# Kernel tuning notes

Measured on AMD Instinct MI355X. Metric: run time of the kernel, lower is better.

Reference implementation:

```python
import jax, jax.numpy as jnp
import numpy as np

B, S, H = 32, 64, 512
ATT = 128


def _window_index_tables(seq_len):
    # Enumerate all contiguous windows of size 2..S, same set (order-independent
    # for the softmax-weighted sum) as the torch double loop.
    starts, ends = [], []
    for w in range(2, seq_len + 1):
        for s in range(0, seq_len - w + 1):
            starts.append(s)
            ends.append(s + w)
    starts = np.asarray(starts, np.int32)
    ends = np.asarray(ends, np.int32)
    widths = ends - starts
    ks = np.floor(np.log2(widths)).astype(np.int32)  # sparse-table level per window
    e2 = ends - (1 << ks)                            # second gather position
    return starts, e2, ks


def setup_inputs() -> dict:
    key = jax.random.key(0)
    k0, k1, k2, k3, k4 = jax.random.split(key, 5)
    return {
        "lstm_out": jax.random.normal(k0, (B, S, H), dtype=jnp.float32),
        "W1": jax.random.normal(k1, (H, ATT), dtype=jnp.float32) * 0.05,
        "b1": jax.random.normal(k2, (ATT,), dtype=jnp.float32) * 0.05,
        "W2": jax.random.normal(k3, (ATT, 1), dtype=jnp.float32) * 0.05,
        "b2": jax.random.normal(k4, (1,), dtype=jnp.float32) * 0.05,
    }


def reference(lstm_out, W1, b1, W2, b2):
    b, s, h = lstm_out.shape
    # Sparse table: M[k][:, i] = max over lstm_out[:, i : i+2^k] (clipped to s).
    n_levels = int(np.floor(np.log2(s))) + 1
    tables = [lstm_out]
    for k in range(1, n_levels):
        half = 1 << (k - 1)
        prev = tables[-1]
        shifted = jnp.concatenate(
            [prev[:, half:], jnp.full((b, half, h), -jnp.inf, prev.dtype)], axis=1)
        tables.append(jnp.maximum(prev, shifted))
    Mstack = jnp.stack(tables)  # [K, B, S, H]

    starts, e2, ks = _window_index_tables(s)
    # Range max of each window = max of two overlapping power-of-two blocks.
    pooled = jnp.maximum(Mstack[ks, :, starts], Mstack[ks, :, e2])  # [n_win, B, H]
    pooled = jnp.transpose(pooled, (1, 0, 2))  # [B, n_win, H]

    hid = jax.nn.relu(jnp.einsum("bnh,ha->bna", pooled, W1) + b1)
    scores = jnp.einsum("bna,ao->bno", hid, W2) + b2  # [B, n_win, 1]
    attn = jax.nn.softmax(scores, axis=1)
    return jnp.sum(attn * pooled, axis=1)  # [B, H]
```

## Files before the change

kernel.cpp:

```cpp
#include <hip/hip_runtime.h>
#include <stdint.h>


typedef unsigned short u16;
typedef unsigned int u32;

#define B_    32
#define S_    64
#define H_    512
#define ATT_  128
#define NWIN  2016
#define NLEV  7
#define TLEV  6

typedef __bf16 bf16x8 __attribute__((ext_vector_type(8)));
typedef float  f32x4  __attribute__((ext_vector_type(4)));

__device__ __forceinline__ float asf(u32 i) {
  union { u32 i; float f; } v; v.i = i; return v.f;
}
__device__ __forceinline__ u32 asu(float f) {
  union { float f; u32 i; } v; v.f = f; return v.i;
}
__device__ __forceinline__ float bf2f(u16 u) { return asf(((u32)u) << 16); }
__device__ __forceinline__ u16 f2bf(float f) {
  u32 i = asu(f);
  i += 0x7fffu + ((i >> 16) & 1u);
  return (u16)(i >> 16);
}
__device__ __forceinline__ u32 bfmax2(u32 a, u32 b) {
  float a0 = asf(a << 16), a1 = asf(a & 0xffff0000u);
  float b0 = asf(b << 16), b1 = asf(b & 0xffff0000u);
  u32 m0 = asu(fmaxf(a0, b0)), m1 = asu(fmaxf(a1, b1));
  return (m1 & 0xffff0000u) | (m0 >> 16);
}
__device__ __forceinline__ uint4 bfmax8(uint4 a, uint4 b) {
  uint4 m;
  m.x = bfmax2(a.x, b.x); m.y = bfmax2(a.y, b.y);
  m.z = bfmax2(a.z, b.z); m.w = bfmax2(a.w, b.w);
  return m;
}
__device__ __forceinline__ bf16x8 as_bf16x8(uint4 v) {
  union { uint4 u; bf16x8 h; } c; c.u = v; return c.h;
}

__launch_bounds__(256)
__global__ void k01_init(const float* __restrict__ lstm, const float* __restrict__ W1,
                         u16* __restrict__ table, u16* __restrict__ w1t,
                         u16* __restrict__ widx) {
  int bid = blockIdx.x, tid = threadIdx.x;
  __shared__ u16 bufA[64 * 64], bufB[64 * 64];
  if (bid < 256) {
    int hc = bid & 7, b = bid >> 3;
    const float* src = lstm + (size_t)b * S_ * H_ + hc * 64;
    u16* tb = table + (size_t)b * TLEV * S_ * H_ + hc * 64;
    for (int t = tid; t < 64 * 16; t += 256) {
      int r = t >> 4, c4 = t & 15;
      float4 f = *reinterpret_cast<const float4*>(src + r * H_ + c4 * 4);
      ushort4 u;
      u.x = f2bf(f.x); u.y = f2bf(f.y); u.z = f2bf(f.z); u.w = f2bf(f.w);
      *reinterpret_cast<ushort4*>(&bufA[r * 64 + c4 * 4]) = u;
    }
    u16* pa = bufA; u16* pb = bufB;
    for (int k = 1; k < NLEV; ++k) {
      __syncthreads();
      int half = 1 << (k - 1);
      u16* dst_g = tb + (size_t)(k - 1) * S_ * H_;
      for (int t = tid; t < 64 * 16; t += 256) {
        int r = t >> 4, c4 = t & 15;
        int r2 = r + half; if (r2 > 63) r2 = 63;
        uint2 a  = *reinterpret_cast<const uint2*>(&pa[r  * 64 + c4 * 4]);
        uint2 bq = *reinterpret_cast<const uint2*>(&pa[r2 * 64 + c4 * 4]);
        uint2 m; m.x = bfmax2(a.x, bq.x); m.y = bfmax2(a.y, bq.y);
        *reinterpret_cast<uint2*>(&pb[r * 64 + c4 * 4]) = m;
        *reinterpret_cast<uint2*>(dst_g + r * H_ + c4 * 4) = m;
      }
      u16* tmp = pa; pa = pb; pb = tmp;
    }
  } else {
    int gb = bid - 256;
    if (gb == 0) {
      for (int n = tid; n < NWIN; n += 256) {
        int w = 2, rem = n;
        while (rem >= 65 - w) { rem -= 65 - w; ++w; }
        int s = rem;
        int k = 31 - __clz(w);
        int e2 = s + w - (1 << k);
        widx[n] = (u16)(s | (e2 << 6) | (k << 12));
      }
    }
    for (int q = tid; q < 2048; q += 256) {
      int idx = gb * 2048 + q;
      int n = idx >> 9, kq = idx & 511;
      w1t[idx] = f2bf(W1[kq * ATT_ + n]);
    }
  }
}

__launch_bounds__(256)
__attribute__((amdgpu_waves_per_eu(1, 4)))
__global__ void k2_scores(const u16* __restrict__ table, const u16* __restrict__ w1t,
                          const float* __restrict__ b1, const float* __restrict__ w2,
                          const u16* __restrict__ widx, float* __restrict__ scores) {
  const int b = blockIdx.y, mt = blockIdx.x;
  __shared__ u16 Ts[128 * 64];
  __shared__ u16 Bs[128 * 64];
  __shared__ u16 widx_l[64];
  __shared__ float b1s[128], w2s[128];
  int tid = threadIdx.x;
  if (tid < 64) {
    int n = mt * 64 + tid; if (n > NWIN - 1) n = NWIN - 1;
    widx_l[tid] = widx[n];
  }
  if (tid < 128) { b1s[tid] = b1[tid]; w2s[tid] = w2[tid]; }
  __syncthreads();

  const int lv_lo = widx_l[0] >> 12;
  const u16* tb = table + (size_t)b * TLEV * S_ * H_ + (size_t)(lv_lo - 1) * S_ * H_;

  int t0 = tid, t1 = tid + 256, t2 = tid + 512, t3 = tid + 768;
  int r0 = t0 >> 3, r1 = t1 >> 3, r2 = t2 >> 3, r3 = t3 >> 3;
  int c0 = t0 & 7,  c1 = t1 & 7,  c2 = t2 & 7,  c3 = t3 & 7;
  const u16* ts0 = tb + r0 * H_ + c0 * 8;
  const u16* ts1 = tb + r1 * H_ + c1 * 8;
  const u16* ts2 = tb + r2 * H_ + c2 * 8;
  const u16* ts3 = tb + r3 * H_ + c3 * 8;
  const u16* bs0 = w1t + r0 * H_ + c0 * 8;
  const u16* bs1 = w1t + r1 * H_ + c1 * 8;
  const u16* bs2 = w1t + r2 * H_ + c2 * 8;
  const u16* bs3 = w1t + r3 * H_ + c3 * 8;
  int sd0 = r0 * 64 + ((c0 ^ (r0 & 7)) * 8);
  int sd1 = r1 * 64 + ((c1 ^ (r1 & 7)) * 8);
  int sd2 = r2 * 64 + ((c2 ^ (r2 & 7)) * 8);
  int sd3 = r3 * 64 + ((c3 ^ (r3 & 7)) * 8);

  int wid = tid >> 6, lane = tid & 63;
  int lrow = lane & 15, quad = lane >> 4;

  int aoff[2][2];
  {
    int pk = widx_l[wid * 16 + lrow];
    int s = pk & 63, e2 = (pk >> 6) & 63, lv = (pk >> 12) - lv_lo;
    int rs = lv * 64 + s, re = lv * 64 + e2;
#pragma unroll
    for (int k2i = 0; k2i < 2; ++k2i) {
      int c = quad + k2i * 4;
      aoff[k2i][0] = rs * 64 + ((c ^ (rs & 7)) * 8);
      aoff[k2i][1] = re * 64 + ((c ^ (re & 7)) * 8);
    }
  }
  int boff[8][2];
#pragma unroll
  for (int j = 0; j < 8; ++j) {
    int n = j * 16 + lrow;
#pragma unroll
    for (int k2i = 0; k2i < 2; ++k2i) {
      int c = quad + k2i * 4;
      boff[j][k2i] = n * 64 + ((c ^ (n & 7)) * 8);
    }
  }

  uint4 rT0, rT1, rT2, rT3, rB0, rB1, rB2, rB3;

#define ISSUE(KK) do { \
  rT0 = *reinterpret_cast<const uint4*>(ts0 + (KK)); \
  rT1 = *reinterpret_cast<const uint4*>(ts1 + (KK)); \
  rT2 = *reinterpret_cast<const uint4*>(ts2 + (KK)); \
  rT3 = *reinterpret_cast<const uint4*>(ts3 + (KK)); \
  rB0 = *reinterpret_cast<const uint4*>(bs0 + (KK)); \
  rB1 = *reinterpret_cast<const uint4*>(bs1 + (KK)); \
  rB2 = *reinterpret_cast<const uint4*>(bs2 + (KK)); \
  rB3 = *reinterpret_cast<const uint4*>(bs3 + (KK)); \
} while (0)

#define STAGE() do { \
  *reinterpret_cast<uint4*>(&Ts[sd0]) = rT0; \
  *reinterpret_cast<uint4*>(&Ts[sd1]) = rT1; \
  *reinterpret_cast<uint4*>(&Ts[sd2]) = rT2; \
  *reinterpret_cast<uint4*>(&Ts[sd3]) = rT3; \
  *reinterpret_cast<uint4*>(&Bs[sd0]) = rB0; \
  *reinterpret_cast<uint4*>(&Bs[sd1]) = rB1; \
  *reinterpret_cast<uint4*>(&Bs[sd2]) = rB2; \
  *reinterpret_cast<uint4*>(&Bs[sd3]) = rB3; \
} while (0)

  ISSUE(0);

  f32x4 acc[8];
#pragma unroll
  for (int j = 0; j < 8; ++j) acc[j] = (f32x4){0.f, 0.f, 0.f, 0.f};

  for (int kc = 0; kc < 7; ++kc) {
    __syncthreads();
    STAGE();
    __syncthreads();
    ISSUE((kc + 1) * 64);
#pragma unroll
    for (int k2i = 0; k2i < 2; ++k2i) {
      uint4 va = *reinterpret_cast<const uint4*>(&Ts[aoff[k2i][0]]);
      uint4 vb = *reinterpret_cast<const uint4*>(&Ts[aoff[k2i][1]]);
      bf16x8 af = as_bf16x8(bfmax8(va, vb));
#pragma unroll
      for (int j = 0; j < 8; ++j) {
        bf16x8 bfr = *reinterpret_cast<const bf16x8*>(&Bs[boff[j][k2i]]);
        acc[j] = __builtin_amdgcn_mfma_f32_16x16x32_bf16(af, bfr, acc[j], 0, 0, 0);
      }
    }
  }
  __syncthreads();
  STAGE();
  __syncthreads();
#pragma unroll
  for (int k2i = 0; k2i < 2; ++k2i) {
    uint4 va = *reinterpret_cast<const uint4*>(&Ts[aoff[k2i][0]]);
    uint4 vb = *reinterpret_cast<const uint4*>(&Ts[aoff[k2i][1]]);
    bf16x8 af = as_bf16x8(bfmax8(va, vb));
#pragma unroll
    for (int j = 0; j < 8; ++j) {
      bf16x8 bfr = *reinterpret_cast<const bf16x8*>(&Bs[boff[j][k2i]]);
      acc[j] = __builtin_amdgcn_mfma_f32_16x16x32_bf16(af, bfr, acc[j], 0, 0, 0);
    }
  }

#undef ISSUE
#undef STAGE

#pragma unroll
  for (int r = 0; r < 4; ++r) {
    float p = 0.f;
#pragma unroll
    for (int j = 0; j < 8; ++j) {
      int n = j * 16 + lrow;
      float v = acc[j][r] + b1s[n];
      p += (v > 0.f ? v : 0.f) * w2s[n];
    }
    p += __shfl_xor(p, 1, 16);
    p += __shfl_xor(p, 2, 16);
    p += __shfl_xor(p, 4, 16);
    p += __shfl_xor(p, 8, 16);
    if (lrow == 0) {
      int nw = mt * 64 + wid * 16 + quad * 4 + r;
      if (nw < NWIN) scores[b * NWIN + nw] = p;
    }
  }
}

__launch_bounds__(256)
__global__ void k34_out(const u16* __restrict__ table, const float* __restrict__ scores,
                        const u16* __restrict__ widx, float* __restrict__ out) {
  int hc = blockIdx.x, b = blockIdx.y, tid = threadIdx.x;
  __shared__ u16 Tl[6 * 64 * 32];
  __shared__ float attn_l[NWIN];
  __shared__ u16 widx_l[NWIN];
  __shared__ float red[8][32];
  __shared__ float wredM[4], wredS[4];
  const u16* tb = table + (size_t)b * TLEV * S_ * H_;
  int h0 = hc * 32;
  int lane = tid & 63, wid = tid >> 6;

  for (int t = tid; t < 6 * 64 * 4; t += 256) {
    int row = t >> 2, c = t & 3;
    uint4 v = *reinterpret_cast<const uint4*>(tb + row * H_ + h0 + c * 8);
    *reinterpret_cast<uint4*>(&Tl[row * 32 + c * 8]) = v;
  }
  for (int n = tid; n < NWIN; n += 256) widx_l[n] = widx[n];

  float mx = -1e30f;
  for (int n = tid; n < NWIN; n += 256) {
    float v = scores[b * NWIN + n];
    attn_l[n] = v;
    mx = fmaxf(mx, v);
  }
#pragma unroll
  for (int off = 32; off > 0; off >>= 1) mx = fmaxf(mx, __shfl_xor(mx, off, 64));
  if (lane == 0) wredM[wid] = mx;
  __syncthreads();
  mx = fmaxf(fmaxf(wredM[0], wredM[1]), fmaxf(wredM[2], wredM[3]));
  float sum = 0.f;
  for (int n = tid; n < NWIN; n += 256) {
    float e = __expf(attn_l[n] - mx);
    attn_l[n] = e;
    sum += e;
  }
#pragma unroll
  for (int off = 32; off > 0; off >>= 1) sum += __shfl_xor(sum, off, 64);
  if (lane == 0) wredS[wid] = sum;
  __syncthreads();
  float inv = 1.f / (wredS[0] + wredS[1] + wredS[2] + wredS[3]);

  int h = tid & 31, g = tid >> 5;
  float acc = 0.f;
  for (int n = g * 252; n < g * 252 + 252; ++n) {
    int pk = widx_l[n];
    int s = pk & 63, e2 = (pk >> 6) & 63, lv = pk >> 12;
    float va = bf2f(Tl[((lv - 1) * 64 + s) * 32 + h]);
    float vb = bf2f(Tl[((lv - 1) * 64 + e2) * 32 + h]);
    acc += attn_l[n] * fmaxf(va, vb);
  }
  red[g][h] = acc;
  __syncthreads();
  if (tid < 32) {
    float s2 = 0.f;
#pragma unroll
    for (int g2 = 0; g2 < 8; ++g2) s2 += red[g2][tid];
    out[b * H_ + h0 + tid] = s2 * inv;
  }
}

extern "C" void kernel_launch(void* const* d_in, const int* in_sizes, int n_in,
                              void* d_out, int out_size, void* d_ws, size_t ws_size,
                              hipStream_t stream) {
  const float* lstm = (const float*)d_in[0];
  const float* W1   = (const float*)d_in[1];
  const float* b1   = (const float*)d_in[2];
  const float* W2   = (const float*)d_in[3];
  float* out = (float*)d_out;

  char* ws = (char*)d_ws;
  u16*   widx   = (u16*)(ws + 0);
  u16*   w1t    = (u16*)(ws + 4096);
  u16*   table  = (u16*)(ws + 135168);
  float* scores = (float*)(ws + 12718080);

  k01_init <<<288, 256, 0, stream>>>(lstm, W1, table, w1t, widx);
  k2_scores<<<dim3(32, B_), 256, 0, stream>>>(table, w1t, b1, W2, widx, scores);
  k34_out  <<<dim3(16, B_), 256, 0, stream>>>(table, scores, widx, out);
}
```

Baseline: 117.6 us.

## Enlarge score GEMM tile to 256 windows with double-buffered direct-to-LDS loads

The scores kernel now has each block cover 256 windows instead of 64. Each wave computes four 16-row M sub-tiles, so every W1 fragment read from shared memory is reused four times, and the block count falls from 32 to 8 per batch. Global-to-register-to-LDS staging is replaced by global_load_lds async copies into double-buffered shared tiles, with one barrier per K step. In exchange the accumulator count per wave grows fourfold and occupancy drops to one block per CU. Correctness relies on the async LDS copies being complete at each barrier, and on any 256-window block spanning at most two sparse-table levels.

```diff
diff --git a/kernel.cpp b/kernel.cpp
--- a/kernel.cpp
+++ b/kernel.cpp
@@ -97,19 +97,18 @@
   }
 }
 
-__launch_bounds__(256)
-__attribute__((amdgpu_waves_per_eu(1, 4)))
+__launch_bounds__(256, 1)
 __global__ void k2_scores(const u16* __restrict__ table, const u16* __restrict__ w1t,
                           const float* __restrict__ b1, const float* __restrict__ w2,
                           const u16* __restrict__ widx, float* __restrict__ scores) {
   const int b = blockIdx.y, mt = blockIdx.x;
-  __shared__ u16 Ts[128 * 64];
-  __shared__ u16 Bs[128 * 64];
-  __shared__ u16 widx_l[64];
+  __shared__ u16 Ts[2][128 * 64];
+  __shared__ u16 Bs[2][128 * 64];
+  __shared__ u16 widx_l[256];
   __shared__ float b1s[128], w2s[128];
   int tid = threadIdx.x;
-  if (tid < 64) {
-    int n = mt * 64 + tid; if (n > NWIN - 1) n = NWIN - 1;
+  {
+    int n = mt * 256 + tid; if (n > NWIN - 1) n = NWIN - 1;
     widx_l[tid] = widx[n];
   }
   if (tid < 128) { b1s[tid] = b1[tid]; w2s[tid] = w2[tid]; }
@@ -118,35 +117,46 @@
   const int lv_lo = widx_l[0] >> 12;
   const u16* tb = table + (size_t)b * TLEV * S_ * H_ + (size_t)(lv_lo - 1) * S_ * H_;
 
-  int t0 = tid, t1 = tid + 256, t2 = tid + 512, t3 = tid + 768;
-  int r0 = t0 >> 3, r1 = t1 >> 3, r2 = t2 >> 3, r3 = t3 >> 3;
-  int c0 = t0 & 7,  c1 = t1 & 7,  c2 = t2 & 7,  c3 = t3 & 7;
-  const u16* ts0 = tb + r0 * H_ + c0 * 8;
-  const u16* ts1 = tb + r1 * H_ + c1 * 8;
-  const u16* ts2 = tb + r2 * H_ + c2 * 8;
-  const u16* ts3 = tb + r3 * H_ + c3 * 8;
-  const u16* bs0 = w1t + r0 * H_ + c0 * 8;
-  const u16* bs1 = w1t + r1 * H_ + c1 * 8;
-  const u16* bs2 = w1t + r2 * H_ + c2 * 8;
-  const u16* bs3 = w1t + r3 * H_ + c3 * 8;
-  int sd0 = r0 * 64 + ((c0 ^ (r0 & 7)) * 8);
-  int sd1 = r1 * 64 + ((c1 ^ (r1 & 7)) * 8);
-  int sd2 = r2 * 64 + ((c2 ^ (r2 & 7)) * 8);
-  int sd3 = r3 * 64 + ((c3 ^ (r3 & 7)) * 8);
+  const u16* gT[4]; const u16* gB[4]; int sl[4];
+#pragma unroll
+  for (int p = 0; p < 4; ++p) {
+    int slot = p * 256 + tid;
+    int r = slot >> 3, c = slot & 7;
+    int csw = (c ^ (r & 7)) * 8;
+    gT[p] = tb  + r * H_ + csw;
+    gB[p] = w1t + r * H_ + csw;
+    sl[p] = slot * 8;
+  }
+
+#define DMA(KC, BSEL) do {                                                     \
+    int ko_ = (KC) * 64;                                                       \
+    _Pragma("unroll")                                                          \
+    for (int p_ = 0; p_ < 4; ++p_) {                                           \
+      __builtin_amdgcn_global_load_lds(                                        \
+          (const __attribute__((address_space(1))) void*)(gT[p_] + ko_),       \
+          (__attribute__((address_space(3))) void*)(&Ts[(BSEL)][sl[p_]]),      \
+          16, 0, 0);                                                           \
+      __builtin_amdgcn_global_load_lds(                                        \
+          (const __attribute__((address_space(1))) void*)(gB[p_] + ko_),       \
+          (__attribute__((address_space(3))) void*)(&Bs[(BSEL)][sl[p_]]),      \
+          16, 0, 0);                                                           \
+    }                                                                          \
+  } while (0)
 
   int wid = tid >> 6, lane = tid & 63;
   int lrow = lane & 15, quad = lane >> 4;
 
-  int aoff[2][2];
-  {
-    int pk = widx_l[wid * 16 + lrow];
+  int aoff[4][2][2];
+#pragma unroll
+  for (int mi = 0; mi < 4; ++mi) {
+    int pk = widx_l[wid * 64 + mi * 16 + lrow];
     int s = pk & 63, e2 = (pk >> 6) & 63, lv = (pk >> 12) - lv_lo;
     int rs = lv * 64 + s, re = lv * 64 + e2;
 #pragma unroll
     for (int k2i = 0; k2i < 2; ++k2i) {
       int c = quad + k2i * 4;
-      aoff[k2i][0] = rs * 64 + ((c ^ (rs & 7)) * 8);
-      aoff[k2i][1] = re * 64 + ((c ^ (re & 7)) * 8);
+      aoff[mi][k2i][0] = rs * 64 + ((c ^ (rs & 7)) * 8);
+      aoff[mi][k2i][1] = re * 64 + ((c ^ (re & 7)) * 8);
     }
   }
   int boff[8][2];
@@ -160,87 +170,57 @@
     }
   }
 
-  uint4 rT0, rT1, rT2, rT3, rB0, rB1, rB2, rB3;
-
-#define ISSUE(KK) do { \
-  rT0 = *reinterpret_cast<const uint4*>(ts0 + (KK)); \
-  rT1 = *reinterpret_cast<const uint4*>(ts1 + (KK)); \
-  rT2 = *reinterpret_cast<const uint4*>(ts2 + (KK)); \
-  rT3 = *reinterpret_cast<const uint4*>(ts3 + (KK)); \
-  rB0 = *reinterpret_cast<const uint4*>(bs0 + (KK)); \
-  rB1 = *reinterpret_cast<const uint4*>(bs1 + (KK)); \
-  rB2 = *reinterpret_cast<const uint4*>(bs2 + (KK)); \
-  rB3 = *reinterpret_cast<const uint4*>(bs3 + (KK)); \
-} while (0)
-
-#define STAGE() do { \
-  *reinterpret_cast<uint4*>(&Ts[sd0]) = rT0; \
-  *reinterpret_cast<uint4*>(&Ts[sd1]) = rT1; \
-  *reinterpret_cast<uint4*>(&Ts[sd2]) = rT2; \
-  *reinterpret_cast<uint4*>(&Ts[sd3]) = rT3; \
-  *reinterpret_cast<uint4*>(&Bs[sd0]) = rB0; \
-  *reinterpret_cast<uint4*>(&Bs[sd1]) = rB1; \
-  *reinterpret_cast<uint4*>(&Bs[sd2]) = rB2; \
-  *reinterpret_cast<uint4*>(&Bs[sd3]) = rB3; \
-} while (0)
-
-  ISSUE(0);
-
-  f32x4 acc[8];
-#pragma unroll
-  for (int j = 0; j < 8; ++j) acc[j] = (f32x4){0.f, 0.f, 0.f, 0.f};
-
-  for (int kc = 0; kc < 7; ++kc) {
+  f32x4 acc[4][8];
+#pragma unroll
+  for (int mi = 0; mi < 4; ++mi)
+#pragma unroll
+    for (int j = 0; j < 8; ++j) acc[mi][j] = (f32x4){0.f, 0.f, 0.f, 0.f};
+
+  DMA(0, 0);
+
+  for (int kc = 0; kc < 8; ++kc) {
     __syncthreads();
-    STAGE();
-    __syncthreads();
-    ISSUE((kc + 1) * 64);
+    if (kc < 7) DMA(kc + 1, (kc + 1) & 1);
+    const u16* Tc = Ts[kc & 1];
+    const u16* Bc = Bs[kc & 1];
 #pragma unroll
     for (int k2i = 0; k2i < 2; ++k2i) {
-      uint4 va = *reinterpret_cast<const uint4*>(&Ts[aoff[k2i][0]]);
-      uint4 vb = *reinterpret_cast<const uint4*>(&Ts[aoff[k2i][1]]);
-      bf16x8 af = as_bf16x8(bfmax8(va, vb));
+      bf16x8 bfr[8];
+#pragma unroll
+      for (int j = 0; j < 8; ++j)
+        bfr[j] = *reinterpret_cast<const bf16x8*>(&Bc[boff[j][k2i]]);
+#pragma unroll
+      for (int mi = 0; mi < 4; ++mi) {
+        uint4 va = *reinterpret_cast<const uint4*>(&Tc[aoff[mi][k2i][0]]);
+        uint4 vb = *reinterpret_cast<const uint4*>(&Tc[aoff[mi][k2i][1]]);
+        bf16x8 af = as_bf16x8(bfmax8(va, vb));
+#pragma unroll
+        for (int j = 0; j < 8; ++j)
+          acc[mi][j] = __builtin_amdgcn_mfma_f32_16x16x32_bf16(af, bfr[j], acc[mi][j], 0, 0, 0);
+      }
+    }
+  }
+#undef DMA
+
+#pragma unroll
+  for (int mi = 0; mi < 4; ++mi) {
+#pragma unroll
+    for (int r = 0; r < 4; ++r) {
+      float p = 0.f;
 #pragma unroll
       for (int j = 0; j < 8; ++j) {
-        bf16x8 bfr = *reinterpret_cast<const bf16x8*>(&Bs[boff[j][k2i]]);
-        acc[j] = __builtin_amdgcn_mfma_f32_16x16x32_bf16(af, bfr, acc[j], 0, 0, 0);
-      }
-    }
-  }
-  __syncthreads();
-  STAGE();
-  __syncthreads();
-#pragma unroll
-  for (int k2i = 0; k2i < 2; ++k2i) {
-    uint4 va = *reinterpret_cast<const uint4*>(&Ts[aoff[k2i][0]]);
-    uint4 vb = *reinterpret_cast<const uint4*>(&Ts[aoff[k2i][1]]);
-    bf16x8 af = as_bf16x8(bfmax8(va, vb));
-#pragma unroll
-    for (int j = 0; j < 8; ++j) {
-      bf16x8 bfr = *reinterpret_cast<const bf16x8*>(&Bs[boff[j][k2i]]);
-      acc[j] = __builtin_amdgcn_mfma_f32_16x16x32_bf16(af, bfr, acc[j], 0, 0, 0);
-    }
-  }
-
-#undef ISSUE
-#undef STAGE
-
-#pragma unroll
-  for (int r = 0; r < 4; ++r) {
-    float p = 0.f;
-#pragma unroll
-    for (int j = 0; j < 8; ++j) {
-      int n = j * 16 + lrow;
-      float v = acc[j][r] + b1s[n];
-      p += (v > 0.f ? v : 0.f) * w2s[n];
-    }
-    p += __shfl_xor(p, 1, 16);
-    p += __shfl_xor(p, 2, 16);
-    p += __shfl_xor(p, 4, 16);
-    p += __shfl_xor(p, 8, 16);
-    if (lrow == 0) {
-      int nw = mt * 64 + wid * 16 + quad * 4 + r;
-      if (nw < NWIN) scores[b * NWIN + nw] = p;
+        int n = j * 16 + lrow;
+        float v = acc[mi][j][r] + b1s[n];
+        p += (v > 0.f ? v : 0.f) * w2s[n];
+      }
+      p += __shfl_xor(p, 1, 16);
+      p += __shfl_xor(p, 2, 16);
+      p += __shfl_xor(p, 4, 16);
+      p += __shfl_xor(p, 8, 16);
+      if (lrow == 0) {
+        int nw = mt * 256 + wid * 64 + mi * 16 + quad * 4 + r;
+        if (nw < NWIN) scores[b * NWIN + nw] = p;
+      }
     }
   }
 }
@@ -323,6 +303,6 @@
   float* scores = (float*)(ws + 12718080);
 
   k01_init <<<288, 256, 0, stream>>>(lstm, W1, table, w1t, widx);
-  k2_scores<<<dim3(32, B_), 256, 0, stream>>>(table, w1t, b1, W2, widx, scores);
+  k2_scores<<<dim3(8, B_), 256, 0, stream>>>(table, w1t, b1, W2, widx, scores);
   k34_out  <<<dim3(16, B_), 256, 0, stream>>>(table, scores, widx, out);
 }
```

Result: no change. 118.8 us (+1.0%).
